# Kernel optimization log

Measured on AMD Instinct MI355X. Metric: run time of the kernel, lower is better.

Reference implementation:

```python
import jax, jax.numpy as jnp
import numpy as np

B, T, H = 128, 2048, 256

def setup_inputs() -> dict:
    key = jax.random.key(0)
    k1, k2, k3 = jax.random.split(key, 3)
    hidden_states = jax.random.normal(k1, (B, T, H), dtype=jnp.float32)
    W_score = jax.random.normal(k2, (H, H), dtype=jnp.float32) / np.sqrt(H)
    W_att = jax.random.normal(k3, (2 * H, 128), dtype=jnp.float32) / np.sqrt(2 * H)
    return {"hidden_states": hidden_states, "W_score": W_score, "W_att": W_att}

def reference(hidden_states, W_score, W_att):
    # score_first_part: (B, T, H)
    score_first_part = jnp.einsum('bth,hk->btk', hidden_states, W_score)
    # last hidden state h_t: (B, H)
    h_t = hidden_states[:, -1, :]
    # attention scores: (B, T)
    score = jnp.einsum('bth,bh->bt', score_first_part, h_t)
    attention_weights = jax.nn.softmax(score, axis=-1)
    # context vector: (B, H)
    context_vector = jnp.einsum('bth,bt->bh', hidden_states, attention_weights)
    pre_activation = jnp.concatenate([context_vector, h_t], axis=-1)  # (B, 2H)
    attention_vector = jnp.tanh(pre_activation @ W_att)  # (B, 128)
    return attention_vector
```

## Files before the change

kernel.cpp:

```cpp
#include <hip/hip_runtime.h>
#include <math.h>

namespace {
constexpr int kB = 128;
constexpr int kT = 2048;
constexpr int kH = 256;
constexpr int kS = 16;
constexpr int kTC = kT / kS;
}

__device__ __forceinline__ float dot4(float4 a, float4 b) {
    return fmaf(a.x, b.x, fmaf(a.y, b.y, fmaf(a.z, b.z, a.w * b.w)));
}

__global__ __launch_bounds__(256) void compute_v_kernel(
    const float* __restrict__ hs, const float* __restrict__ Wsc,
    float* __restrict__ v) {
    const int b = blockIdx.x;
    const int tid = threadIdx.x;
    __shared__ float sh[kH];
    sh[tid] = hs[(size_t)b * kT * kH + (size_t)(kT - 1) * kH + tid];
    __syncthreads();
    const int wv = tid >> 6, lane = tid & 63;
    const float4 hv = *reinterpret_cast<const float4*>(&sh[lane * 4]);
    for (int r = 0; r < 64; ++r) {
        const int h = wv * 64 + r;
        const float4 wr =
            *reinterpret_cast<const float4*>(&Wsc[(size_t)h * kH + lane * 4]);
        float s = dot4(wr, hv);
        #pragma unroll
        for (int off = 32; off > 0; off >>= 1) s += __shfl_xor(s, off, 64);
        if (lane == 0) v[b * kH + h] = s;
    }
}

__global__ __launch_bounds__(256) void main_pass_kernel(
    const float* __restrict__ hs, const float* __restrict__ v,
    float* __restrict__ M, float* __restrict__ L, float* __restrict__ CTX) {
    const int chunk = blockIdx.x;
    const int b = blockIdx.y;
    const int tid = threadIdx.x;
    const int wv = tid >> 6, lane = tid & 63;

    const float4 vv = *reinterpret_cast<const float4*>(&v[b * kH + lane * 4]);
    const float* base = hs + (size_t)b * kT * kH + (size_t)chunk * kTC * kH;

    float m = -INFINITY, l = 0.f;
    float4 acc = make_float4(0.f, 0.f, 0.f, 0.f);

    #pragma unroll 2
    for (int it = 0; it < kTC / 16; ++it) {
        const float* p = base + (size_t)(it * 16 + wv * 4) * kH + lane * 4;
        const float4 x0 = *reinterpret_cast<const float4*>(p);
        const float4 x1 = *reinterpret_cast<const float4*>(p + kH);
        const float4 x2 = *reinterpret_cast<const float4*>(p + 2 * kH);
        const float4 x3 = *reinterpret_cast<const float4*>(p + 3 * kH);
        float s0 = dot4(x0, vv);
        float s1 = dot4(x1, vv);
        float s2 = dot4(x2, vv);
        float s3 = dot4(x3, vv);
        #pragma unroll
        for (int off = 32; off > 0; off >>= 1) {
            s0 += __shfl_xor(s0, off, 64);
            s1 += __shfl_xor(s1, off, 64);
            s2 += __shfl_xor(s2, off, 64);
            s3 += __shfl_xor(s3, off, 64);
        }
        const float nm =
            fmaxf(fmaxf(m, fmaxf(s0, s1)), fmaxf(s2, s3));
        const float scale = __expf(m - nm);
        const float p0 = __expf(s0 - nm);
        const float p1 = __expf(s1 - nm);
        const float p2 = __expf(s2 - nm);
        const float p3 = __expf(s3 - nm);
        l = fmaf(l, scale, (p0 + p1) + (p2 + p3));
        acc.x = fmaf(acc.x, scale,
                     fmaf(p0, x0.x, fmaf(p1, x1.x, fmaf(p2, x2.x, p3 * x3.x))));
        acc.y = fmaf(acc.y, scale,
                     fmaf(p0, x0.y, fmaf(p1, x1.y, fmaf(p2, x2.y, p3 * x3.y))));
        acc.z = fmaf(acc.z, scale,
                     fmaf(p0, x0.z, fmaf(p1, x1.z, fmaf(p2, x2.z, p3 * x3.z))));
        acc.w = fmaf(acc.w, scale,
                     fmaf(p0, x0.w, fmaf(p1, x1.w, fmaf(p2, x2.w, p3 * x3.w))));
        m = nm;
    }

    __shared__ float shm[4];
    __shared__ float shl[4];
    __shared__ float shctx[4 * kH];
    if (lane == 0) { shm[wv] = m; shl[wv] = l; }
    *reinterpret_cast<float4*>(&shctx[wv * kH + lane * 4]) = acc;
    __syncthreads();

    const float m0 = shm[0], m1 = shm[1], m2 = shm[2], m3 = shm[3];
    const float gm = fmaxf(fmaxf(m0, m1), fmaxf(m2, m3));
    const float e0 = __expf(m0 - gm), e1 = __expf(m1 - gm);
    const float e2 = __expf(m2 - gm), e3 = __expf(m3 - gm);

    const int pidx = b * kS + chunk;
    const float ctx = shctx[tid] * e0 + shctx[kH + tid] * e1 +
                      shctx[2 * kH + tid] * e2 + shctx[3 * kH + tid] * e3;
    CTX[(size_t)pidx * kH + tid] = ctx;
    if (tid == 0) {
        M[pidx] = gm;
        L[pidx] = shl[0] * e0 + shl[1] * e1 + shl[2] * e2 + shl[3] * e3;
    }
}

__global__ __launch_bounds__(256) void finalize_kernel(
    const float* __restrict__ hs, const float* __restrict__ M,
    const float* __restrict__ L, const float* __restrict__ CTX,
    const float* __restrict__ Watt, float* __restrict__ out) {
    const int b = blockIdx.x;
    const int tid = threadIdx.x;
    __shared__ float pre[2 * kH];
    __shared__ float red[128];

    float gm = -INFINITY;
    #pragma unroll
    for (int c = 0; c < kS; ++c) gm = fmaxf(gm, M[b * kS + c]);
    float gl = 0.f, ctx = 0.f;
    #pragma unroll
    for (int c = 0; c < kS; ++c) {
        const float e = __expf(M[b * kS + c] - gm);
        gl = fmaf(L[b * kS + c], e, gl);
        ctx = fmaf(CTX[(size_t)(b * kS + c) * kH + tid], e, ctx);
    }
    pre[tid] = ctx / gl;
    pre[kH + tid] = hs[(size_t)b * kT * kH + (size_t)(kT - 1) * kH + tid];
    __syncthreads();

    const int j = tid & 127, half = tid >> 7;
    float s = 0.f;
    const int i0 = half * 256;
    #pragma unroll 4
    for (int i = i0; i < i0 + 256; ++i)
        s = fmaf(pre[i], Watt[(size_t)i * 128 + j], s);
    if (half == 1) red[j] = s;
    __syncthreads();
    if (half == 0) out[b * 128 + j] = tanhf(s + red[j]);
}

extern "C" void kernel_launch(void* const* d_in, const int* in_sizes, int n_in,
                              void* d_out, int out_size, void* d_ws, size_t ws_size,
                              hipStream_t stream) {
    const float* hs   = (const float*)d_in[0];
    const float* Wsc  = (const float*)d_in[1];
    const float* Watt = (const float*)d_in[2];
    float* out = (float*)d_out;

    float* ws  = (float*)d_ws;
    float* v   = ws;
    float* M   = v + kB * kH;
    float* L   = M + kB * kS;
    float* CTX = L + kB * kS;

    compute_v_kernel<<<kB, 256, 0, stream>>>(hs, Wsc, v);
    main_pass_kernel<<<dim3(kS, kB), 256, 0, stream>>>(hs, v, M, L, CTX);
    finalize_kernel<<<kB, 256, 0, stream>>>(hs, M, L, CTX, Watt, out);
}
```

Baseline: 423.7 us.

## Use DPP wave reductions, deepen per-wave row batch, split v computation

```diff
diff --git a/kernel.cpp b/kernel.cpp
--- a/kernel.cpp
+++ b/kernel.cpp
@@ -13,23 +13,40 @@
     return fmaf(a.x, b.x, fmaf(a.y, b.y, fmaf(a.z, b.z, a.w * b.w)));
 }
 
+template <int CTRL, int ROW_MASK>
+__device__ __forceinline__ float dpp_add(float x) {
+    int n = __builtin_amdgcn_update_dpp(0, __float_as_int(x), CTRL, ROW_MASK,
+                                        0xf, true);
+    return x + __int_as_float(n);
+}
+
+__device__ __forceinline__ float wave_sum(float x) {
+    x = dpp_add<0xB1, 0xf>(x);
+    x = dpp_add<0x4E, 0xf>(x);
+    x = dpp_add<0x141, 0xf>(x);
+    x = dpp_add<0x140, 0xf>(x);
+    x = dpp_add<0x142, 0xa>(x);
+    x = dpp_add<0x143, 0xc>(x);
+    return __int_as_float(__builtin_amdgcn_readlane(__float_as_int(x), 63));
+}
+
 __global__ __launch_bounds__(256) void compute_v_kernel(
     const float* __restrict__ hs, const float* __restrict__ Wsc,
     float* __restrict__ v) {
-    const int b = blockIdx.x;
+    const int half = blockIdx.x;
+    const int b = blockIdx.y;
     const int tid = threadIdx.x;
     __shared__ float sh[kH];
     sh[tid] = hs[(size_t)b * kT * kH + (size_t)(kT - 1) * kH + tid];
     __syncthreads();
     const int wv = tid >> 6, lane = tid & 63;
     const float4 hv = *reinterpret_cast<const float4*>(&sh[lane * 4]);
-    for (int r = 0; r < 64; ++r) {
-        const int h = wv * 64 + r;
+    #pragma unroll 4
+    for (int r = 0; r < 32; ++r) {
+        const int h = half * 128 + wv * 32 + r;
         const float4 wr =
             *reinterpret_cast<const float4*>(&Wsc[(size_t)h * kH + lane * 4]);
-        float s = dot4(wr, hv);
-        #pragma unroll
-        for (int off = 32; off > 0; off >>= 1) s += __shfl_xor(s, off, 64);
+        const float s = wave_sum(dot4(wr, hv));
         if (lane == 0) v[b * kH + h] = s;
     }
 }
@@ -48,40 +65,37 @@
     float m = -INFINITY, l = 0.f;
     float4 acc = make_float4(0.f, 0.f, 0.f, 0.f);
 
-    #pragma unroll 2
-    for (int it = 0; it < kTC / 16; ++it) {
-        const float* p = base + (size_t)(it * 16 + wv * 4) * kH + lane * 4;
-        const float4 x0 = *reinterpret_cast<const float4*>(p);
-        const float4 x1 = *reinterpret_cast<const float4*>(p + kH);
-        const float4 x2 = *reinterpret_cast<const float4*>(p + 2 * kH);
-        const float4 x3 = *reinterpret_cast<const float4*>(p + 3 * kH);
-        float s0 = dot4(x0, vv);
-        float s1 = dot4(x1, vv);
-        float s2 = dot4(x2, vv);
-        float s3 = dot4(x3, vv);
+    for (int it = 0; it < kTC / 32; ++it) {
+        const float* p = base + (size_t)(it * 32 + wv * 8) * kH + lane * 4;
+        float4 x[8];
         #pragma unroll
-        for (int off = 32; off > 0; off >>= 1) {
-            s0 += __shfl_xor(s0, off, 64);
-            s1 += __shfl_xor(s1, off, 64);
-            s2 += __shfl_xor(s2, off, 64);
-            s3 += __shfl_xor(s3, off, 64);
+        for (int j = 0; j < 8; ++j)
+            x[j] = *reinterpret_cast<const float4*>(p + j * kH);
+        float s[8];
+        #pragma unroll
+        for (int j = 0; j < 8; ++j) s[j] = wave_sum(dot4(x[j], vv));
+
+        float nm = m;
+        #pragma unroll
+        for (int j = 0; j < 8; ++j) nm = fmaxf(nm, s[j]);
+        const float scale = __expf(m - nm);
+        float pj[8], psum = 0.f;
+        #pragma unroll
+        for (int j = 0; j < 8; ++j) { pj[j] = __expf(s[j] - nm); psum += pj[j]; }
+        l = fmaf(l, scale, psum);
+
+        float ix = 0.f, iy = 0.f, iz = 0.f, iw = 0.f;
+        #pragma unroll
+        for (int j = 0; j < 8; ++j) {
+            ix = fmaf(pj[j], x[j].x, ix);
+            iy = fmaf(pj[j], x[j].y, iy);
+            iz = fmaf(pj[j], x[j].z, iz);
+            iw = fmaf(pj[j], x[j].w, iw);
         }
-        const float nm =
-            fmaxf(fmaxf(m, fmaxf(s0, s1)), fmaxf(s2, s3));
-        const float scale = __expf(m - nm);
-        const float p0 = __expf(s0 - nm);
-        const float p1 = __expf(s1 - nm);
-        const float p2 = __expf(s2 - nm);
-        const float p3 = __expf(s3 - nm);
-        l = fmaf(l, scale, (p0 + p1) + (p2 + p3));
-        acc.x = fmaf(acc.x, scale,
-                     fmaf(p0, x0.x, fmaf(p1, x1.x, fmaf(p2, x2.x, p3 * x3.x))));
-        acc.y = fmaf(acc.y, scale,
-                     fmaf(p0, x0.y, fmaf(p1, x1.y, fmaf(p2, x2.y, p3 * x3.y))));
-        acc.z = fmaf(acc.z, scale,
-                     fmaf(p0, x0.z, fmaf(p1, x1.z, fmaf(p2, x2.z, p3 * x3.z))));
-        acc.w = fmaf(acc.w, scale,
-                     fmaf(p0, x0.w, fmaf(p1, x1.w, fmaf(p2, x2.w, p3 * x3.w))));
+        acc.x = fmaf(acc.x, scale, ix);
+        acc.y = fmaf(acc.y, scale, iy);
+        acc.z = fmaf(acc.z, scale, iz);
+        acc.w = fmaf(acc.w, scale, iw);
         m = nm;
     }
 
@@ -155,7 +169,7 @@
     float* L   = M + kB * kS;
     float* CTX = L + kB * kS;
 
-    compute_v_kernel<<<kB, 256, 0, stream>>>(hs, Wsc, v);
+    compute_v_kernel<<<dim3(2, kB), 256, 0, stream>>>(hs, Wsc, v);
     main_pass_kernel<<<dim3(kS, kB), 256, 0, stream>>>(hs, v, M, L, CTX);
     finalize_kernel<<<kB, 256, 0, stream>>>(hs, M, L, CTX, Watt, out);
 }
```

New measurement: 399.5 us. -5.7%, faster.
